# Optimization experiments

Measured on AMD Instinct MI355X. Metric: run time of the kernel, lower is better.

## Reference

```python
import jax, jax.numpy as jnp
import numpy as np

A_NUM = 9
C_NUM = 20


def generate_anchor(anc, grid):
    # anc: (A,2) w,h ; grid: (B,H,W,2) centers -> anchors (B,A,H,W,4)
    centers = grid[:, None]                      # (B,1,H,W,2)
    half = anc.reshape(1, -1, 1, 1, 2) * 0.5     # (1,A,1,1,2)
    return jnp.concatenate([centers - half, centers + half], axis=-1)


def iou_matrix(proposals, bboxes):
    # proposals: (B,A,H,W,4) -> (B,K,4); bboxes: (B,N,5)
    B = proposals.shape[0]
    p = proposals.reshape(B, -1, 4)[:, :, None, :]   # (B,K,1,4)
    bb = bboxes[:, None, :, :]                       # (B,1,N,5)
    s_p = (p[..., 2] - p[..., 0]) * (p[..., 3] - p[..., 1])
    s_b = (bb[..., 2] - bb[..., 0]) * (bb[..., 3] - bb[..., 1])
    ix1 = jnp.maximum(p[..., 0], bb[..., 0])
    iy1 = jnp.maximum(p[..., 1], bb[..., 1])
    ix2 = jnp.minimum(p[..., 2], bb[..., 2])
    iy2 = jnp.minimum(p[..., 3], bb[..., 3])
    s_i = jnp.clip(ix2 - ix1, 0.0) * jnp.clip(iy2 - iy1, 0.0)
    s_u = s_p + s_b - s_i
    iou = jnp.clip(s_i / (s_u + 1e-8), 0.0)
    invalid = (s_u <= 0) | (s_p <= 0) | (s_b <= 0) | (bb[..., 0] < 0)
    return jnp.where(invalid, 0.0, iou)              # (B,K,N)


def extract_anchor_data(anchor_data, idx):
    # anchor_data: (B,A,D,H,W) -> flat (B*A*H*W, D) -> gather
    B, A, D, H, W = anchor_data.shape
    flat = jnp.transpose(anchor_data, (0, 1, 3, 4, 2)).reshape(-1, D)
    return flat[idx]


def extract_class_scores(all_scores, idx, num_anchors):
    # all_scores: (B,C,H,W) -> (B,A,H,W,C) flat -> gather
    B, C, H, W = all_scores.shape
    s = jnp.transpose(all_scores, (0, 2, 3, 1))[:, None]          # (B,1,H,W,C)
    s = jnp.broadcast_to(s, (B, num_anchors, H, W, C)).reshape(-1, C)
    return s[idx]


def setup_inputs() -> dict:
    key = jax.random.key(0)
    ks = jax.random.split(key, 8)
    B, Cin, H, W = 32, 1280, 28, 28
    N, M = 64, 4096
    hid, out_ch = 128, 5 * A_NUM + C_NUM
    features = jax.random.normal(ks[0], (B, Cin, H, W), dtype=jnp.float32)
    # grid of feature-cell centers (GenerateGrid-style)
    xs = jnp.arange(W, dtype=jnp.float32) + 0.5
    ys = jnp.arange(H, dtype=jnp.float32) + 0.5
    gx, gy = jnp.meshgrid(xs, ys, indexing='xy')
    grid = jnp.broadcast_to(jnp.stack([gx, gy], axis=-1), (B, H, W, 2))
    anc = jnp.array([[1.0, 1], [2, 2], [3, 3], [4, 4], [5, 5], [2, 3], [3, 2], [3, 5], [5, 3]], dtype=jnp.float32)
    tl = jax.random.uniform(ks[1], (B, N, 2), minval=0.0, maxval=20.0)
    wh = jax.random.uniform(ks[2], (B, N, 2), minval=1.0, maxval=8.0)
    cls = jax.random.randint(ks[3], (B, N, 1), 0, C_NUM).astype(jnp.float32)
    bb = jnp.concatenate([tl, tl + wh, cls], axis=-1)
    valid = jax.random.uniform(ks[4], (B, N, 1)) > 0.25
    bboxes = jnp.where(valid, bb, -1.0)
    K = B * A_NUM * H * W
    pos_anchor_idx = jax.random.randint(ks[5], (M,), 0, K, dtype=jnp.int64 if jax.config.jax_enable_x64 else jnp.int32)
    neg_anchor_idx = jax.random.randint(ks[6], (M,), 0, K, dtype=pos_anchor_idx.dtype)
    W1 = jax.random.normal(ks[7], (hid, Cin), dtype=jnp.float32) * 0.02
    b1 = jnp.zeros((hid,), dtype=jnp.float32)
    W2 = jax.random.normal(jax.random.fold_in(key, 99), (out_ch, hid), dtype=jnp.float32) * 0.02
    b2 = jnp.zeros((out_ch,), dtype=jnp.float32)
    return {"features": features, "grid": grid, "anc": anc, "bboxes": bboxes,
            "pos_anchor_idx": pos_anchor_idx, "neg_anchor_idx": neg_anchor_idx,
            "W1": W1, "b1": b1, "W2": W2, "b2": b2}


def reference(features, grid, anc, bboxes, pos_anchor_idx, neg_anchor_idx, W1, b1, W2, b2):
    B, Cin, H, W = features.shape
    A, C = A_NUM, C_NUM
    # anchors + broadcast IoU matrix
    anchors = generate_anchor(anc, grid)                 # (B,A,H,W,4)
    iou_mat = iou_matrix(anchors, bboxes)                # (B,A*H*W,N)
    # prediction head: 1x1 conv -> (dropout eval: identity) -> leaky_relu -> 1x1 conv
    h = jnp.einsum('bchw,oc->bohw', features, W1) + b1[None, :, None, None]
    h = jax.nn.leaky_relu(h, negative_slope=0.01)
    out = jnp.einsum('bchw,oc->bohw', h, W2) + b2[None, :, None, None]  # (B,5A+C,H,W)
    anchor_raw = out[:, :5 * A].reshape(B, A, 5, H, W)
    conf_sq = jax.nn.sigmoid(anchor_raw[:, :, 0:1])      # (B,A,1,H,W)
    off_raw = anchor_raw[:, :, 1:]                       # (B,A,4,H,W)
    off_sq = jnp.concatenate([jax.nn.sigmoid(off_raw[:, :, :2]) - 0.5, off_raw[:, :, 2:]], axis=2)
    class_raw = out[:, 5 * A:]                           # (B,C,H,W)
    # training path: irregular gathers
    class_scores = extract_class_scores(class_raw, pos_anchor_idx, A)   # (M,C)
    offsets = extract_anchor_data(off_sq, pos_anchor_idx)               # (M,4)
    conf_pos = extract_anchor_data(conf_sq, pos_anchor_idx)             # (M,1)
    conf_neg = extract_anchor_data(conf_sq, neg_anchor_idx)             # (M,1)
    conf_scores = jnp.concatenate([conf_pos, conf_neg], axis=0)         # (2M,1)
    return conf_scores, offsets, class_scores, iou_mat
```

## Files before the change

kernel.cpp:

```cpp
#include <hip/hip_runtime.h>
#include <cstdint>

#define A_NUM 9
#define C_NUM 20
#define B_SZ 32
#define HW 784
#define P_NUM (A_NUM*HW)
#define NBOX 64
#define CIN 1280
#define HID 128
#define M_IDX 4096
#define KSPLIT 4
#define KS_PER 10
#define ASTR 40
#define PSTR ((size_t)B_SZ * HW * HID)
#define IOU_PB 64

#define CONF_OFF 0
#define OFFS_OFF (2*M_IDX)
#define CLS_OFF  (OFFS_OFF + 4*M_IDX)
#define IOU_OFF  (CLS_OFF + C_NUM*M_IDX)

typedef short bf16x8 __attribute__((ext_vector_type(8)));
typedef float f32x4  __attribute__((ext_vector_type(4)));

__device__ __forceinline__ unsigned pack_bf16(float lo, float hi) {
  unsigned a = __builtin_bit_cast(unsigned, lo);
  unsigned b = __builtin_bit_cast(unsigned, hi);
  return ((a + 0x8000u) >> 16) | ((b + 0x8000u) & 0xffff0000u);
}

__global__ __launch_bounds__(256) void prep_w1(const float* __restrict__ W1,
                                               uint4* __restrict__ W1f) {
  int id = blockIdx.x * 256 + threadIdx.x;
  int lane = id & 63;
  int ntile = (id >> 6) & 7;
  int ks = id >> 9;
  int lo = lane & 15, quad = lane >> 4;
  int n = ntile * 16 + lo;
  int k0 = ks * 32 + quad * 8;
  const float* src = W1 + n * CIN + k0;
  float4 x = *(const float4*)src;
  float4 y = *(const float4*)(src + 4);
  uint4 p;
  p.x = pack_bf16(x.x, x.y);
  p.y = pack_bf16(x.z, x.w);
  p.z = pack_bf16(y.x, y.y);
  p.w = pack_bf16(y.z, y.w);
  W1f[id] = p;
}

__global__ __launch_bounds__(256) void gemm1_mfma(
    const float* __restrict__ F, const unsigned short* __restrict__ W1f,
    float* __restrict__ Part) {
  __shared__ unsigned short Asm[2][64 * ASTR];

  const int b = blockIdx.y;
  const int z = blockIdx.z;
  const int m0 = blockIdx.x * 64;
  const int t = threadIdx.x;
  const int wave = t >> 6, lane = t & 63;
  const int quad = lane >> 4, lo = lane & 15;
  const int ksbase = z * KS_PER;

  const int sm = t & 63;
  const int kh = t >> 6;
  const int gm = m0 + sm;
  const bool mval = gm < HW;
  const float* Fb = F + (size_t)b * CIN * HW + (mval ? gm : 0);

  f32x4 acc[4][2];
#pragma unroll
  for (int i = 0; i < 4; i++)
#pragma unroll
    for (int j = 0; j < 2; j++) acc[i][j] = (f32x4){0.f, 0.f, 0.f, 0.f};

  float va[8];
  uint4 vb[2][2];

  auto loadA = [&](int kk) {
    const int k0 = (ksbase + kk) * 32 + kh * 8;
#pragma unroll
    for (int i = 0; i < 8; i++) va[i] = Fb[(size_t)(k0 + i) * HW];
  };
  auto loadB = [&](int kk, uint4* dst) {
    const unsigned short* g =
        W1f + (size_t)(((ksbase + kk) * 8 + wave * 2) * 64 + lane) * 8;
    dst[0] = *(const uint4*)g;
    dst[1] = *(const uint4*)(g + 512);
  };
  auto stageA = [&](int buf) {
    uint4 p;
    if (mval) {
      p.x = pack_bf16(va[0], va[1]);
      p.y = pack_bf16(va[2], va[3]);
      p.z = pack_bf16(va[4], va[5]);
      p.w = pack_bf16(va[6], va[7]);
    } else {
      p = (uint4){0, 0, 0, 0};
    }
    *(uint4*)&Asm[buf][sm * ASTR + kh * 8] = p;
  };
  auto compute = [&](int buf, uint4* bv) {
    const unsigned short* Ab = &Asm[buf][lo * ASTR + quad * 8];
    bf16x8 af[4];
#pragma unroll
    for (int i = 0; i < 4; i++) af[i] = *(const bf16x8*)(Ab + i * 16 * ASTR);
    bf16x8 b0 = __builtin_bit_cast(bf16x8, bv[0]);
    bf16x8 b1 = __builtin_bit_cast(bf16x8, bv[1]);
#pragma unroll
    for (int i = 0; i < 4; i++) {
      acc[i][0] = __builtin_amdgcn_mfma_f32_16x16x32_bf16(af[i], b0, acc[i][0], 0, 0, 0);
      acc[i][1] = __builtin_amdgcn_mfma_f32_16x16x32_bf16(af[i], b1, acc[i][1], 0, 0, 0);
    }
  };

  loadA(0);
  loadB(0, vb[0]);
  stageA(0);
  __syncthreads();
  for (int kk = 0; kk < KS_PER; kk++) {
    const int cur = kk & 1;
    if (kk + 1 < KS_PER) {
      loadA(kk + 1);
      loadB(kk + 1, vb[cur ^ 1]);
    }
    compute(cur, vb[cur]);
    if (kk + 1 < KS_PER) stageA(cur ^ 1);
    __syncthreads();
  }

  float* Pz = Part + ((size_t)(z * B_SZ + b) * HW) * HID;
#pragma unroll
  for (int i = 0; i < 4; i++) {
    const int mbase = m0 + i * 16 + quad * 4;
#pragma unroll
    for (int j = 0; j < 2; j++) {
      const int n = wave * 32 + j * 16 + lo;
#pragma unroll
      for (int r = 0; r < 4; r++) {
        const int mm = mbase + r;
        if (mm < HW) Pz[(size_t)mm * HID + n] = acc[i][j][r];
      }
    }
  }
}

__global__ __launch_bounds__(256) void iou_kernel(
    const float* __restrict__ grid, const float* __restrict__ anc,
    const float* __restrict__ bboxes, float* __restrict__ out) {
  __shared__ float sb[NBOX * 5];
  __shared__ float4 sp4[IOU_PB];
  const int b = blockIdx.y;
  const int p0 = blockIdx.x * IOU_PB;
  const int t = threadIdx.x;
  for (int i = t; i < NBOX * 5; i += 256) sb[i] = bboxes[b * NBOX * 5 + i];
  if (t < IOU_PB) {
    int p = p0 + t;
    float x1 = 0.f, y1 = 0.f, x2 = 0.f, y2 = 0.f;
    if (p < P_NUM) {
      int a = p / HW, hw = p - a * HW;
      float2 c = ((const float2*)grid)[b * HW + hw];
      float hx = anc[a * 2 + 0] * 0.5f, hy = anc[a * 2 + 1] * 0.5f;
      x1 = c.x - hx; y1 = c.y - hy; x2 = c.x + hx; y2 = c.y + hy;
    }
    sp4[t] = make_float4(x1, y1, x2, y2);
  }
  __syncthreads();
  const int nl = (t & 15) * 4;
  const int pi = t >> 4;
#pragma unroll
  for (int ip = 0; ip < 4; ip++) {
    const int pl = pi + 16 * ip;
    const int p = p0 + pl;
    const float4 pb = sp4[pl];
    const float spA = (pb.z - pb.x) * (pb.w - pb.y);
    float4 res;
#pragma unroll
    for (int jn = 0; jn < 4; jn++) {
      const int n = nl + jn;
      float bx1 = sb[n * 5 + 0], by1 = sb[n * 5 + 1];
      float bx2 = sb[n * 5 + 2], by2 = sb[n * 5 + 3];
      float s_b = (bx2 - bx1) * (by2 - by1);
      float ix1 = fmaxf(pb.x, bx1), iy1 = fmaxf(pb.y, by1);
      float ix2 = fminf(pb.z, bx2), iy2 = fminf(pb.w, by2);
      float si = fmaxf(ix2 - ix1, 0.f) * fmaxf(iy2 - iy1, 0.f);
      float su = spA + s_b - si;
      float iou = fmaxf(si / (su + 1e-8f), 0.f);
      bool invalid = (su <= 0.f) | (spA <= 0.f) | (s_b <= 0.f) | (bx1 < 0.f);
      float v = invalid ? 0.f : iou;
      if (jn == 0) res.x = v; else if (jn == 1) res.y = v;
      else if (jn == 2) res.z = v; else res.w = v;
    }
    if (p < P_NUM)
      *(float4*)&out[((size_t)(b * P_NUM + p)) * 64 + nl] = res;
  }
}

__global__ __launch_bounds__(256) void gather_kernel(
    const int* __restrict__ pos_idx, const int* __restrict__ neg_idx,
    const float* __restrict__ Part, const float* __restrict__ b1,
    const float* __restrict__ W2, const float* __restrict__ b2,
    float* __restrict__ out) {
  __shared__ float sh[4][HID];
  const int sub = threadIdx.x >> 6;
  const int l = threadIdx.x & 63;
  const int blk = blockIdx.x * 4 + sub;
  const bool pos = blk < M_IDX;
  const int idx = pos ? pos_idx[blk] : neg_idx[blk - M_IDX];
  const int b = idx / P_NUM;
  const int r = idx - b * P_NUM;
  const int a = r / HW;
  const int hw = r - a * HW;
  const float2* row = (const float2*)(Part + ((size_t)(b * HW + hw)) * HID) + l;
  float2 s0 = row[0];
  float2 s1 = row[PSTR / 2];
  float2 s2 = row[2 * (PSTR / 2)];
  float2 s3 = row[3 * (PSTR / 2)];
  float v0 = s0.x + s1.x + s2.x + s3.x + b1[2 * l];
  float v1 = s0.y + s1.y + s2.y + s3.y + b1[2 * l + 1];
  v0 = v0 > 0.f ? v0 : 0.01f * v0;
  v1 = v1 > 0.f ? v1 : 0.01f * v1;
  sh[sub][2 * l] = v0; sh[sub][2 * l + 1] = v1;
  __syncthreads();
  if (pos) {
    if (l < 25) {
      int o = (l < 5) ? (a * 5 + l) : (5 * A_NUM + (l - 5));
      const float* w = W2 + o * HID;
      float dot = b2[o];
#pragma unroll 8
      for (int k = 0; k < HID; k++) dot = fmaf(w[k], sh[sub][k], dot);
      if (l == 0) {
        out[CONF_OFF + blk] = 1.f / (1.f + expf(-dot));
      } else if (l < 3) {
        out[OFFS_OFF + blk * 4 + (l - 1)] = 1.f / (1.f + expf(-dot)) - 0.5f;
      } else if (l < 5) {
        out[OFFS_OFF + blk * 4 + (l - 1)] = dot;
      } else {
        out[CLS_OFF + blk * C_NUM + (l - 5)] = dot;
      }
    }
  } else {
    int o = a * 5;
    const float* w = W2 + o * HID;
    float part = fmaf(w[2 * l], v0, w[2 * l + 1] * v1);
#pragma unroll
    for (int off = 32; off > 0; off >>= 1) part += __shfl_down(part, off);
    if (l == 0) out[CONF_OFF + blk] = 1.f / (1.f + expf(-(b2[o] + part)));
  }
}

extern "C" void kernel_launch(void* const* d_in, const int* in_sizes, int n_in,
                              void* d_out, int out_size, void* d_ws, size_t ws_size,
                              hipStream_t stream) {
  const float* features = (const float*)d_in[0];
  const float* grid     = (const float*)d_in[1];
  const float* anc      = (const float*)d_in[2];
  const float* bboxes   = (const float*)d_in[3];
  const int*   pos_idx  = (const int*)d_in[4];
  const int*   neg_idx  = (const int*)d_in[5];
  const float* W1       = (const float*)d_in[6];
  const float* b1       = (const float*)d_in[7];
  const float* W2       = (const float*)d_in[8];
  const float* b2       = (const float*)d_in[9];
  float* out = (float*)d_out;

  uint4* W1f = (uint4*)d_ws;
  float* Part = (float*)((char*)d_ws + 327680);

  hipLaunchKernelGGL(prep_w1, dim3(80), dim3(256), 0, stream, W1, W1f);
  hipLaunchKernelGGL(gemm1_mfma, dim3(13, B_SZ, KSPLIT), dim3(256), 0, stream,
                     features, (const unsigned short*)W1f, Part);
  hipLaunchKernelGGL(iou_kernel, dim3((P_NUM + IOU_PB - 1) / IOU_PB, B_SZ),
                     dim3(256), 0, stream, grid, anc, bboxes, out + IOU_OFF);
  hipLaunchKernelGGL(gather_kernel, dim3(2 * M_IDX / 4), dim3(256),
                     0, stream, pos_idx, neg_idx, Part, b1, W2, b2, out);
}
```

Before: 261.5 us.

## Fuse full-K GEMM1 with head GEMM2 epilogue and IoU into one kernel

Removes the 4-way K split, so each block runs the full K=1280 reduction. Its epilogue then applies bias and leaky ReLU, stages the hidden tile in LDS as bf16, and runs the second 1x1 conv with MFMA against pre-packed W2, writing an 80-wide activated head output. IoU blocks are merged into the same launch, and the gather becomes a plain copy from that output. This avoids writing and re-reading four fp32 partial hidden tensors and the per-index dot products, but it cuts GEMM parallelism by 4x and rounds the hidden activations to bf16.

```diff
diff --git a/kernel.cpp b/kernel.cpp
--- a/kernel.cpp
+++ b/kernel.cpp
@@ -10,10 +10,10 @@
 #define CIN 1280
 #define HID 128
 #define M_IDX 4096
-#define KSPLIT 4
-#define KS_PER 10
+#define KS_ALL 40
 #define ASTR 40
-#define PSTR ((size_t)B_SZ * HW * HID)
+#define HSTR 136
+#define OSTR 80
 #define IOU_PB 64
 
 #define CONF_OFF 0
@@ -21,6 +21,10 @@
 #define CLS_OFF  (OFFS_OFF + 4*M_IDX)
 #define IOU_OFF  (CLS_OFF + C_NUM*M_IDX)
 
+#define GEMM_BLKS (13*B_SZ)
+#define IOU_BX ((P_NUM + IOU_PB - 1)/IOU_PB)
+#define IOU_BLKS (IOU_BX*B_SZ)
+
 typedef short bf16x8 __attribute__((ext_vector_type(8)));
 typedef float f32x4  __attribute__((ext_vector_type(4)));
 
@@ -30,38 +34,119 @@
   return ((a + 0x8000u) >> 16) | ((b + 0x8000u) & 0xffff0000u);
 }
 
-__global__ __launch_bounds__(256) void prep_w1(const float* __restrict__ W1,
-                                               uint4* __restrict__ W1f) {
+__global__ __launch_bounds__(256) void prep_w(const float* __restrict__ W1,
+                                              const float* __restrict__ W2,
+                                              uint4* __restrict__ W1f,
+                                              uint4* __restrict__ W2f) {
   int id = blockIdx.x * 256 + threadIdx.x;
-  int lane = id & 63;
-  int ntile = (id >> 6) & 7;
-  int ks = id >> 9;
-  int lo = lane & 15, quad = lane >> 4;
-  int n = ntile * 16 + lo;
-  int k0 = ks * 32 + quad * 8;
-  const float* src = W1 + n * CIN + k0;
-  float4 x = *(const float4*)src;
-  float4 y = *(const float4*)(src + 4);
-  uint4 p;
-  p.x = pack_bf16(x.x, x.y);
-  p.y = pack_bf16(x.z, x.w);
-  p.z = pack_bf16(y.x, y.y);
-  p.w = pack_bf16(y.z, y.w);
-  W1f[id] = p;
-}
-
-__global__ __launch_bounds__(256) void gemm1_mfma(
+  if (id < 20480) {
+    int lane = id & 63;
+    int ntile = (id >> 6) & 7;
+    int ks = id >> 9;
+    int lo = lane & 15, quad = lane >> 4;
+    int n = ntile * 16 + lo;
+    int k0 = ks * 32 + quad * 8;
+    const float* src = W1 + n * CIN + k0;
+    float4 x = *(const float4*)src;
+    float4 y = *(const float4*)(src + 4);
+    uint4 p;
+    p.x = pack_bf16(x.x, x.y);
+    p.y = pack_bf16(x.z, x.w);
+    p.z = pack_bf16(y.x, y.y);
+    p.w = pack_bf16(y.z, y.w);
+    W1f[id] = p;
+  } else {
+    int i2 = id - 20480;
+    int lane = i2 & 63;
+    int ntile = (i2 >> 6) % 5;
+    int ks = i2 / 320;
+    int lo = lane & 15, quad = lane >> 4;
+    int n = ntile * 16 + lo;
+    int k0 = ks * 32 + quad * 8;
+    uint4 p = (uint4){0, 0, 0, 0};
+    if (n < 5 * A_NUM + C_NUM) {
+      const float* src = W2 + n * HID + k0;
+      float4 x = *(const float4*)src;
+      float4 y = *(const float4*)(src + 4);
+      p.x = pack_bf16(x.x, x.y);
+      p.y = pack_bf16(x.z, x.w);
+      p.z = pack_bf16(y.x, y.y);
+      p.w = pack_bf16(y.z, y.w);
+    }
+    W2f[i2] = p;
+  }
+}
+
+union SharedU {
+  struct { unsigned short Asm[2][64 * ASTR]; } g;
+  struct { unsigned short hs[64 * HSTR]; } e;
+  struct { float sb[NBOX * 5]; float4 sp4[IOU_PB]; } i;
+};
+
+__global__ __launch_bounds__(256) void fused_main(
     const float* __restrict__ F, const unsigned short* __restrict__ W1f,
-    float* __restrict__ Part) {
-  __shared__ unsigned short Asm[2][64 * ASTR];
-
-  const int b = blockIdx.y;
-  const int z = blockIdx.z;
-  const int m0 = blockIdx.x * 64;
+    const unsigned short* __restrict__ W2f, const float* __restrict__ b1,
+    const float* __restrict__ b2, float* __restrict__ Hd,
+    const float* __restrict__ gridc, const float* __restrict__ anc,
+    const float* __restrict__ bboxes, float* __restrict__ iou_out) {
+  __shared__ SharedU sh;
+  const int bid = blockIdx.x;
   const int t = threadIdx.x;
+
+  if (bid >= GEMM_BLKS) {
+    const int bid2 = bid - GEMM_BLKS;
+    const int b = bid2 / IOU_BX;
+    const int p0 = (bid2 - b * IOU_BX) * IOU_PB;
+    float* sb = sh.i.sb;
+    float4* sp4 = sh.i.sp4;
+    for (int i = t; i < NBOX * 5; i += 256) sb[i] = bboxes[b * NBOX * 5 + i];
+    if (t < IOU_PB) {
+      int p = p0 + t;
+      float x1 = 0.f, y1 = 0.f, x2 = 0.f, y2 = 0.f;
+      if (p < P_NUM) {
+        int a = p / HW, hw = p - a * HW;
+        float2 c = ((const float2*)gridc)[b * HW + hw];
+        float hx = anc[a * 2 + 0] * 0.5f, hy = anc[a * 2 + 1] * 0.5f;
+        x1 = c.x - hx; y1 = c.y - hy; x2 = c.x + hx; y2 = c.y + hy;
+      }
+      sp4[t] = make_float4(x1, y1, x2, y2);
+    }
+    __syncthreads();
+    const int nl = (t & 15) * 4;
+    const int pi = t >> 4;
+#pragma unroll
+    for (int ip = 0; ip < 4; ip++) {
+      const int pl = pi + 16 * ip;
+      const int p = p0 + pl;
+      const float4 pb = sp4[pl];
+      const float spA = (pb.z - pb.x) * (pb.w - pb.y);
+      float4 res;
+#pragma unroll
+      for (int jn = 0; jn < 4; jn++) {
+        const int n = nl + jn;
+        float bx1 = sb[n * 5 + 0], by1 = sb[n * 5 + 1];
+        float bx2 = sb[n * 5 + 2], by2 = sb[n * 5 + 3];
+        float s_b = (bx2 - bx1) * (by2 - by1);
+        float ix1 = fmaxf(pb.x, bx1), iy1 = fmaxf(pb.y, by1);
+        float ix2 = fminf(pb.z, bx2), iy2 = fminf(pb.w, by2);
+        float si = fmaxf(ix2 - ix1, 0.f) * fmaxf(iy2 - iy1, 0.f);
+        float su = spA + s_b - si;
+        float iou = fmaxf(si / (su + 1e-8f), 0.f);
+        bool invalid = (su <= 0.f) | (spA <= 0.f) | (s_b <= 0.f) | (bx1 < 0.f);
+        float v = invalid ? 0.f : iou;
+        if (jn == 0) res.x = v; else if (jn == 1) res.y = v;
+        else if (jn == 2) res.z = v; else res.w = v;
+      }
+      if (p < P_NUM)
+        *(float4*)&iou_out[((size_t)(b * P_NUM + p)) * 64 + nl] = res;
+    }
+    return;
+  }
+
+  const int b = bid / 13;
+  const int m0 = (bid - b * 13) * 64;
   const int wave = t >> 6, lane = t & 63;
   const int quad = lane >> 4, lo = lane & 15;
-  const int ksbase = z * KS_PER;
 
   const int sm = t & 63;
   const int kh = t >> 6;
@@ -79,13 +164,13 @@
   uint4 vb[2][2];
 
   auto loadA = [&](int kk) {
-    const int k0 = (ksbase + kk) * 32 + kh * 8;
+    const int k0 = kk * 32 + kh * 8;
 #pragma unroll
     for (int i = 0; i < 8; i++) va[i] = Fb[(size_t)(k0 + i) * HW];
   };
   auto loadB = [&](int kk, uint4* dst) {
     const unsigned short* g =
-        W1f + (size_t)(((ksbase + kk) * 8 + wave * 2) * 64 + lane) * 8;
+        W1f + (size_t)((kk * 8 + wave * 2) * 64 + lane) * 8;
     dst[0] = *(const uint4*)g;
     dst[1] = *(const uint4*)(g + 512);
   };
@@ -99,19 +184,19 @@
     } else {
       p = (uint4){0, 0, 0, 0};
     }
-    *(uint4*)&Asm[buf][sm * ASTR + kh * 8] = p;
+    *(uint4*)&sh.g.Asm[buf][sm * ASTR + kh * 8] = p;
   };
   auto compute = [&](int buf, uint4* bv) {
-    const unsigned short* Ab = &Asm[buf][lo * ASTR + quad * 8];
+    const unsigned short* Ab = &sh.g.Asm[buf][lo * ASTR + quad * 8];
     bf16x8 af[4];
 #pragma unroll
     for (int i = 0; i < 4; i++) af[i] = *(const bf16x8*)(Ab + i * 16 * ASTR);
     bf16x8 b0 = __builtin_bit_cast(bf16x8, bv[0]);
-    bf16x8 b1 = __builtin_bit_cast(bf16x8, bv[1]);
+    bf16x8 b1v = __builtin_bit_cast(bf16x8, bv[1]);
 #pragma unroll
     for (int i = 0; i < 4; i++) {
       acc[i][0] = __builtin_amdgcn_mfma_f32_16x16x32_bf16(af[i], b0, acc[i][0], 0, 0, 0);
-      acc[i][1] = __builtin_amdgcn_mfma_f32_16x16x32_bf16(af[i], b1, acc[i][1], 0, 0, 0);
+      acc[i][1] = __builtin_amdgcn_mfma_f32_16x16x32_bf16(af[i], b1v, acc[i][1], 0, 0, 0);
     }
   };
 
@@ -119,134 +204,99 @@
   loadB(0, vb[0]);
   stageA(0);
   __syncthreads();
-  for (int kk = 0; kk < KS_PER; kk++) {
+  for (int kk = 0; kk < KS_ALL; kk++) {
     const int cur = kk & 1;
-    if (kk + 1 < KS_PER) {
+    if (kk + 1 < KS_ALL) {
       loadA(kk + 1);
       loadB(kk + 1, vb[cur ^ 1]);
     }
     compute(cur, vb[cur]);
-    if (kk + 1 < KS_PER) stageA(cur ^ 1);
+    if (kk + 1 < KS_ALL) stageA(cur ^ 1);
     __syncthreads();
   }
 
-  float* Pz = Part + ((size_t)(z * B_SZ + b) * HW) * HID;
-#pragma unroll
-  for (int i = 0; i < 4; i++) {
-    const int mbase = m0 + i * 16 + quad * 4;
-#pragma unroll
-    for (int j = 0; j < 2; j++) {
-      const int n = wave * 32 + j * 16 + lo;
-#pragma unroll
-      for (int r = 0; r < 4; r++) {
-        const int mm = mbase + r;
-        if (mm < HW) Pz[(size_t)mm * HID + n] = acc[i][j][r];
-      }
-    }
-  }
-}
-
-__global__ __launch_bounds__(256) void iou_kernel(
-    const float* __restrict__ grid, const float* __restrict__ anc,
-    const float* __restrict__ bboxes, float* __restrict__ out) {
-  __shared__ float sb[NBOX * 5];
-  __shared__ float4 sp4[IOU_PB];
-  const int b = blockIdx.y;
-  const int p0 = blockIdx.x * IOU_PB;
-  const int t = threadIdx.x;
-  for (int i = t; i < NBOX * 5; i += 256) sb[i] = bboxes[b * NBOX * 5 + i];
-  if (t < IOU_PB) {
-    int p = p0 + t;
-    float x1 = 0.f, y1 = 0.f, x2 = 0.f, y2 = 0.f;
-    if (p < P_NUM) {
-      int a = p / HW, hw = p - a * HW;
-      float2 c = ((const float2*)grid)[b * HW + hw];
-      float hx = anc[a * 2 + 0] * 0.5f, hy = anc[a * 2 + 1] * 0.5f;
-      x1 = c.x - hx; y1 = c.y - hy; x2 = c.x + hx; y2 = c.y + hy;
-    }
-    sp4[t] = make_float4(x1, y1, x2, y2);
+  {
+    const float bias0 = b1[wave * 32 + lo];
+    const float bias1 = b1[wave * 32 + 16 + lo];
+    unsigned short* hs = sh.e.hs;
+#pragma unroll
+    for (int i = 0; i < 4; i++) {
+#pragma unroll
+      for (int j = 0; j < 2; j++) {
+        const int n = wave * 32 + j * 16 + lo;
+        const float bias = j ? bias1 : bias0;
+#pragma unroll
+        for (int r = 0; r < 4; r++) {
+          float v = acc[i][j][r] + bias;
+          v = v > 0.f ? v : 0.01f * v;
+          const int m = i * 16 + quad * 4 + r;
+          unsigned u = __builtin_bit_cast(unsigned, v);
+          hs[m * HSTR + n] = (unsigned short)((u + 0x8000u) >> 16);
+        }
+      }
+    }
   }
   __syncthreads();
-  const int nl = (t & 15) * 4;
-  const int pi = t >> 4;
-#pragma unroll
-  for (int ip = 0; ip < 4; ip++) {
-    const int pl = pi + 16 * ip;
-    const int p = p0 + pl;
-    const float4 pb = sp4[pl];
-    const float spA = (pb.z - pb.x) * (pb.w - pb.y);
-    float4 res;
-#pragma unroll
-    for (int jn = 0; jn < 4; jn++) {
-      const int n = nl + jn;
-      float bx1 = sb[n * 5 + 0], by1 = sb[n * 5 + 1];
-      float bx2 = sb[n * 5 + 2], by2 = sb[n * 5 + 3];
-      float s_b = (bx2 - bx1) * (by2 - by1);
-      float ix1 = fmaxf(pb.x, bx1), iy1 = fmaxf(pb.y, by1);
-      float ix2 = fminf(pb.z, bx2), iy2 = fminf(pb.w, by2);
-      float si = fmaxf(ix2 - ix1, 0.f) * fmaxf(iy2 - iy1, 0.f);
-      float su = spA + s_b - si;
-      float iou = fmaxf(si / (su + 1e-8f), 0.f);
-      bool invalid = (su <= 0.f) | (spA <= 0.f) | (s_b <= 0.f) | (bx1 < 0.f);
-      float v = invalid ? 0.f : iou;
-      if (jn == 0) res.x = v; else if (jn == 1) res.y = v;
-      else if (jn == 2) res.z = v; else res.w = v;
-    }
-    if (p < P_NUM)
-      *(float4*)&out[((size_t)(b * P_NUM + p)) * 64 + nl] = res;
-  }
-}
-
-__global__ __launch_bounds__(256) void gather_kernel(
+
+  {
+    f32x4 acc2[5];
+#pragma unroll
+    for (int nt = 0; nt < 5; nt++) acc2[nt] = (f32x4){0.f, 0.f, 0.f, 0.f};
+    const unsigned short* hb = sh.e.hs + (wave * 16 + lo) * HSTR + quad * 8;
+#pragma unroll
+    for (int ks = 0; ks < 4; ks++) {
+      bf16x8 af = *(const bf16x8*)(hb + ks * 32);
+#pragma unroll
+      for (int nt = 0; nt < 5; nt++) {
+        bf16x8 bf = *(const bf16x8*)(W2f + (size_t)((ks * 5 + nt) * 64 + lane) * 8);
+        acc2[nt] = __builtin_amdgcn_mfma_f32_16x16x32_bf16(af, bf, acc2[nt], 0, 0, 0);
+      }
+    }
+    const int mrow = m0 + wave * 16 + quad * 4;
+#pragma unroll
+    for (int nt = 0; nt < 5; nt++) {
+      const int o = nt * 16 + lo;
+      if (o < 5 * A_NUM + C_NUM) {
+        const float bz = b2[o];
+        const int t5 = (o < 5 * A_NUM) ? (o % 5) : 5;
+#pragma unroll
+        for (int r = 0; r < 4; r++) {
+          const int m = mrow + r;
+          if (m < HW) {
+            float v = acc2[nt][r] + bz;
+            if (t5 == 0) v = 1.f / (1.f + expf(-v));
+            else if (t5 == 1 || t5 == 2) v = 1.f / (1.f + expf(-v)) - 0.5f;
+            Hd[((size_t)b * HW + m) * OSTR + o] = v;
+          }
+        }
+      }
+    }
+  }
+}
+
+__global__ __launch_bounds__(256) void gather2(
     const int* __restrict__ pos_idx, const int* __restrict__ neg_idx,
-    const float* __restrict__ Part, const float* __restrict__ b1,
-    const float* __restrict__ W2, const float* __restrict__ b2,
-    float* __restrict__ out) {
-  __shared__ float sh[4][HID];
-  const int sub = threadIdx.x >> 6;
-  const int l = threadIdx.x & 63;
-  const int blk = blockIdx.x * 4 + sub;
-  const bool pos = blk < M_IDX;
-  const int idx = pos ? pos_idx[blk] : neg_idx[blk - M_IDX];
-  const int b = idx / P_NUM;
-  const int r = idx - b * P_NUM;
-  const int a = r / HW;
-  const int hw = r - a * HW;
-  const float2* row = (const float2*)(Part + ((size_t)(b * HW + hw)) * HID) + l;
-  float2 s0 = row[0];
-  float2 s1 = row[PSTR / 2];
-  float2 s2 = row[2 * (PSTR / 2)];
-  float2 s3 = row[3 * (PSTR / 2)];
-  float v0 = s0.x + s1.x + s2.x + s3.x + b1[2 * l];
-  float v1 = s0.y + s1.y + s2.y + s3.y + b1[2 * l + 1];
-  v0 = v0 > 0.f ? v0 : 0.01f * v0;
-  v1 = v1 > 0.f ? v1 : 0.01f * v1;
-  sh[sub][2 * l] = v0; sh[sub][2 * l + 1] = v1;
-  __syncthreads();
-  if (pos) {
-    if (l < 25) {
-      int o = (l < 5) ? (a * 5 + l) : (5 * A_NUM + (l - 5));
-      const float* w = W2 + o * HID;
-      float dot = b2[o];
-#pragma unroll 8
-      for (int k = 0; k < HID; k++) dot = fmaf(w[k], sh[sub][k], dot);
-      if (l == 0) {
-        out[CONF_OFF + blk] = 1.f / (1.f + expf(-dot));
-      } else if (l < 3) {
-        out[OFFS_OFF + blk * 4 + (l - 1)] = 1.f / (1.f + expf(-dot)) - 0.5f;
-      } else if (l < 5) {
-        out[OFFS_OFF + blk * 4 + (l - 1)] = dot;
-      } else {
-        out[CLS_OFF + blk * C_NUM + (l - 5)] = dot;
-      }
-    }
+    const float* __restrict__ Hd, float* __restrict__ out) {
+  const int bid = blockIdx.x;
+  if (bid < M_IDX / 8) {
+    const int g = threadIdx.x >> 5;
+    const int l = threadIdx.x & 31;
+    const int slot = bid * 8 + g;
+    const int idx = pos_idx[slot];
+    const int b = idx / P_NUM, r = idx - b * P_NUM;
+    const int a = r / HW, hw = r - a * HW;
+    const float* row = Hd + ((size_t)b * HW + hw) * OSTR;
+    if (l == 0)       out[CONF_OFF + slot] = row[a * 5];
+    else if (l < 5)   out[OFFS_OFF + slot * 4 + (l - 1)] = row[a * 5 + l];
+    else if (l < 25)  out[CLS_OFF + slot * C_NUM + (l - 5)] = row[5 * A_NUM + (l - 5)];
   } else {
-    int o = a * 5;
-    const float* w = W2 + o * HID;
-    float part = fmaf(w[2 * l], v0, w[2 * l + 1] * v1);
-#pragma unroll
-    for (int off = 32; off > 0; off >>= 1) part += __shfl_down(part, off);
-    if (l == 0) out[CONF_OFF + blk] = 1.f / (1.f + expf(-(b2[o] + part)));
+    const int tt = (bid - M_IDX / 8) * 256 + threadIdx.x;
+    if (tt < M_IDX) {
+      const int idx = neg_idx[tt];
+      const int b = idx / P_NUM, r = idx - b * P_NUM;
+      const int a = r / HW, hw = r - a * HW;
+      out[CONF_OFF + M_IDX + tt] = Hd[((size_t)b * HW + hw) * OSTR + a * 5];
+    }
   }
 }
 
@@ -254,7 +304,7 @@
                               void* d_out, int out_size, void* d_ws, size_t ws_size,
                               hipStream_t stream) {
   const float* features = (const float*)d_in[0];
-  const float* grid     = (const float*)d_in[1];
+  const float* gridc    = (const float*)d_in[1];
   const float* anc      = (const float*)d_in[2];
   const float* bboxes   = (const float*)d_in[3];
   const int*   pos_idx  = (const int*)d_in[4];
@@ -266,13 +316,14 @@
   float* out = (float*)d_out;
 
   uint4* W1f = (uint4*)d_ws;
-  float* Part = (float*)((char*)d_ws + 327680);
-
-  hipLaunchKernelGGL(prep_w1, dim3(80), dim3(256), 0, stream, W1, W1f);
-  hipLaunchKernelGGL(gemm1_mfma, dim3(13, B_SZ, KSPLIT), dim3(256), 0, stream,
-                     features, (const unsigned short*)W1f, Part);
-  hipLaunchKernelGGL(iou_kernel, dim3((P_NUM + IOU_PB - 1) / IOU_PB, B_SZ),
-                     dim3(256), 0, stream, grid, anc, bboxes, out + IOU_OFF);
-  hipLaunchKernelGGL(gather_kernel, dim3(2 * M_IDX / 4), dim3(256),
-                     0, stream, pos_idx, neg_idx, Part, b1, W2, b2, out);
-}
+  uint4* W2f = (uint4*)((char*)d_ws + 327680);
+  float* Hd  = (float*)((char*)d_ws + 327680 + 20480);
+
+  hipLaunchKernelGGL(prep_w, dim3(85), dim3(256), 0, stream, W1, W2, W1f, W2f);
+  hipLaunchKernelGGL(fused_main, dim3(GEMM_BLKS + IOU_BLKS), dim3(256), 0, stream,
+                     features, (const unsigned short*)W1f,
+                     (const unsigned short*)W2f, b1, b2, Hd,
+                     gridc, anc, bboxes, out + IOU_OFF);
+  hipLaunchKernelGGL(gather2, dim3(M_IDX / 8 + 16), dim3(256), 0, stream,
+                     pos_idx, neg_idx, Hd, out);
+}
```

New measurement: 284.3 us. +8.7%, slower.
